# Kernel optimization log

Hardware: AMD Instinct MI355X
Metric: run time of the kernel (lower is better)

## Reference

```python
import jax, jax.numpy as jnp
import numpy as np

D = 1024      # features
C = 768       # context dim
H = 16        # heads
HD = D // H   # head dim = 64
N = 2048      # query tokens
M = 2048      # context tokens
EPS = 1e-12
SCALE = float(np.sqrt(HD))


def layernorm(x, w, b):
    c = x - x.mean(axis=-1, keepdims=True)
    s = (c * c).mean(axis=-1, keepdims=True)
    return c * jax.lax.rsqrt(s + EPS) * w + b


def setup_inputs() -> dict:
    key = jax.random.key(0)
    ks = jax.random.split(key, 10)
    sc = 0.02
    return {
        "x": jax.random.normal(ks[0], (N, D), jnp.float32),
        "ctx": jax.random.normal(ks[1], (M, C), jnp.float32),
        # attention projections (Projection: normal*0.02, zero bias)
        "wq": jax.random.normal(ks[2], (D, D), jnp.float32) * sc,
        "bq": jnp.zeros((D,), jnp.float32),
        "wk": jax.random.normal(ks[3], (C, D), jnp.float32) * sc,
        "bk": jnp.zeros((D,), jnp.float32),
        "wv": jax.random.normal(ks[4], (C, D), jnp.float32) * sc,
        "bv": jnp.zeros((D,), jnp.float32),
        "wo": jax.random.normal(ks[5], (D, D), jnp.float32) * sc,
        "bo": jnp.zeros((D,), jnp.float32),
        # MLP
        "w1": jax.random.normal(ks[6], (D, 4 * D), jnp.float32) * sc,
        "b1": jnp.zeros((4 * D,), jnp.float32),
        "w2": jax.random.normal(ks[7], (4 * D, D), jnp.float32) * sc,
        "b2": jnp.zeros((D,), jnp.float32),
        # layernorms
        "qn_w": jnp.ones((D,), jnp.float32), "qn_b": jnp.zeros((D,), jnp.float32),
        "kvn_w": jnp.ones((C,), jnp.float32), "kvn_b": jnp.zeros((C,), jnp.float32),
        "pn_w": jnp.ones((D,), jnp.float32), "pn_b": jnp.zeros((D,), jnp.float32),
    }


def reference(x, ctx, wq, bq, wk, bk, wv, bv, wo, bo, w1, b1, w2, b2,
              qn_w, qn_b, kvn_w, kvn_b, pn_w, pn_b):
    # pre-norm cross-attention
    xq = layernorm(x, qn_w, qn_b)          # [n, d]
    kv = layernorm(ctx, kvn_w, kvn_b)      # [m, c]
    q = (xq @ wq + bq).reshape(N, H, HD).transpose(1, 0, 2)   # [h, n, hd]
    k = (kv @ wk + bk).reshape(M, H, HD).transpose(1, 0, 2)   # [h, m, hd]
    v = (kv @ wv + bv).reshape(M, H, HD).transpose(1, 0, 2)   # [h, m, hd]
    attn = jax.nn.softmax(jnp.einsum('hnd,hmd->hnm', q, k) / SCALE, axis=-1)
    o = jnp.einsum('hnm,hmd->hnd', attn, v).transpose(1, 0, 2).reshape(N, D)
    x = (o @ wo + bo) + x
    # MLP block
    h = layernorm(x, pn_w, pn_b)
    h = jax.nn.gelu(h @ w1 + b1) @ w2 + b2
    return h + x
```

## Files before the change

### kernel.cpp

```cpp
#include <hip/hip_runtime.h>

typedef __bf16 bf16;
typedef __bf16 bf16x4 __attribute__((ext_vector_type(4)));
typedef __bf16 bf16x8 __attribute__((ext_vector_type(8)));
typedef float f32x4 __attribute__((ext_vector_type(4)));

#define N_TOK 2048
#define M_TOK 2048
#define DIM 1024
#define CDIM 768
#define DFF 4096

static __device__ __forceinline__ void async16(const void* g, void* l) {
  __builtin_amdgcn_global_load_lds((const __attribute__((address_space(1))) void*)g,
                                   (__attribute__((address_space(3))) void*)l, 16, 0, 0);
}

__global__ __launch_bounds__(256) void detect_kernel(const void* x, int* flag) {
  __shared__ int cnt;
  if (threadIdx.x == 0) cnt = 0;
  __syncthreads();
  const unsigned* w = (const unsigned*)x;
  int ok = 0;
  for (int i = threadIdx.x; i < 512; i += 256) {
    unsigned lo = w[i] & 0xFFFFu;
    float f = __uint_as_float(lo << 16);
    if (lo == 0u || (fabsf(f) > 1e-3f && fabsf(f) < 1e3f)) ok++;
  }
  atomicAdd(&cnt, ok);
  __syncthreads();
  if (threadIdx.x == 0) *flag = (cnt >= 256) ? 1 : 0;
}

struct ConvArgs {
  const void* src[12];
  bf16* dst[12];
  int n[12];
};
__global__ __launch_bounds__(256) void conv_small_kernel(ConvArgs a, const int* flag) {
  const bool isbf = (*flag != 0);
  const int b = blockIdx.x;
  const void* in = a.src[b];
  bf16* out = a.dst[b];
  const int n = a.n[b];
  for (int i = threadIdx.x; i < n; i += 256)
    out[i] = isbf ? ((const bf16*)in)[i] : (bf16)((const float*)in)[i];
}

struct TmArgs {
  const void* src[4];
  bf16* dst[4];
  int r0[4], Rcnt[4], c0[4], Cfull[4], gx[4], gy[4];
  int force_bf;
};
__global__ __launch_bounds__(256) void tmulti_kernel(TmArgs a, const int* flag) {
  const int z = blockIdx.z;
  if ((int)blockIdx.x >= a.gx[z] || (int)blockIdx.y >= a.gy[z]) return;
  __shared__ bf16 t[32][33];
  const bool isbf = a.force_bf || (*flag != 0);
  const void* in = a.src[z];
  bf16* out = a.dst[z];
  const int Rcnt = a.Rcnt[z], Cfull = a.Cfull[z];
  const int cb = blockIdx.x * 32, rb = blockIdx.y * 32;
  const int tx = threadIdx.x & 31, ty = threadIdx.x >> 5;
#pragma unroll
  for (int i = 0; i < 4; i++) {
    const size_t r = (size_t)(a.r0[z] + rb + ty + i * 8);
    const size_t c = (size_t)(a.c0[z] + cb + tx);
    float v = isbf ? (float)((const bf16*)in)[r * Cfull + c]
                   : ((const float*)in)[r * Cfull + c];
    t[ty + i * 8][tx] = (bf16)v;
  }
  __syncthreads();
#pragma unroll
  for (int i = 0; i < 4; i++)
    out[(size_t)(cb + ty + i * 8) * Rcnt + rb + tx] = t[tx][ty + i * 8];
}

__global__ __launch_bounds__(256) void ln_pair_kernel(
    const void* __restrict__ x0, const bf16* w0, const bf16* b0, bf16* o0,
    const void* __restrict__ x1, const bf16* w1, const bf16* b1, bf16* o1,
    const int* flag) {
  const bool isbf = (*flag != 0);
  const int cols = (blockIdx.y == 0) ? DIM : CDIM;
  const void* x = (blockIdx.y == 0) ? x0 : x1;
  const bf16* w = (blockIdx.y == 0) ? w0 : w1;
  const bf16* b = (blockIdx.y == 0) ? b0 : b1;
  bf16* outp = (blockIdx.y == 0) ? o0 : o1;
  const int row = blockIdx.x;
  const bf16* xr_b = (const bf16*)x + (size_t)row * cols;
  const float* xr_f = (const float*)x + (size_t)row * cols;
  bf16* orow = outp + (size_t)row * cols;
  float s = 0.f, ss = 0.f;
  for (int c = threadIdx.x; c < cols; c += 256) {
    float v = isbf ? (float)xr_b[c] : xr_f[c];
    s += v; ss += v * v;
  }
  for (int d = 1; d < 64; d <<= 1) { s += __shfl_xor(s, d, 64); ss += __shfl_xor(ss, d, 64); }
  __shared__ float sh[8];
  const int wv = threadIdx.x >> 6, lane = threadIdx.x & 63;
  if (lane == 0) { sh[wv] = s; sh[4 + wv] = ss; }
  __syncthreads();
  s = sh[0] + sh[1] + sh[2] + sh[3];
  ss = sh[4] + sh[5] + sh[6] + sh[7];
  const float mean = s / cols;
  float var = ss / cols - mean * mean;
  var = fmaxf(var, 0.f);
  const float r = rsqrtf(var + 1e-12f);
  for (int c = threadIdx.x; c < cols; c += 256) {
    float v = isbf ? (float)xr_b[c] : xr_f[c];
    orow[c] = (bf16)((v - mean) * r * (float)w[c] + (float)b[c]);
  }
}

__global__ __launch_bounds__(256) void ln_kernel(
    const bf16* __restrict__ x, const bf16* __restrict__ w, const bf16* __restrict__ b,
    bf16* __restrict__ out, int cols) {
  const int row = blockIdx.x;
  const bf16* xr = x + (size_t)row * cols;
  bf16* orow = out + (size_t)row * cols;
  float s = 0.f, ss = 0.f;
  for (int c = threadIdx.x; c < cols; c += 256) {
    float v = (float)xr[c];
    s += v; ss += v * v;
  }
  for (int d = 1; d < 64; d <<= 1) { s += __shfl_xor(s, d, 64); ss += __shfl_xor(ss, d, 64); }
  __shared__ float sh[8];
  const int wv = threadIdx.x >> 6, lane = threadIdx.x & 63;
  if (lane == 0) { sh[wv] = s; sh[4 + wv] = ss; }
  __syncthreads();
  s = sh[0] + sh[1] + sh[2] + sh[3];
  ss = sh[4] + sh[5] + sh[6] + sh[7];
  const float mean = s / cols;
  float var = ss / cols - mean * mean;
  var = fmaxf(var, 0.f);
  const float r = rsqrtf(var + 1e-12f);
  for (int c = threadIdx.x; c < cols; c += 256) {
    float v = (float)xr[c];
    orow[c] = (bf16)((v - mean) * r * (float)w[c] + (float)b[c]);
  }
}

__device__ __forceinline__ float gelu_f(float x) {
  float u = 0.7978845608028654f * (x + 0.044715f * x * x * x);
  return 0.5f * x * (1.f + tanhf(u));
}

template <int EPI>
__global__ __launch_bounds__(256) void gemm64(
    const bf16* __restrict__ A, const bf16* __restrict__ Bt,
    const bf16* __restrict__ bias, const void* __restrict__ resid,
    void* __restrict__ Cout, int K, int ldc, const int* flag) {
  __shared__ __align__(16) bf16 As[4][64 * 32];
  __shared__ __align__(16) bf16 Bs[4][64 * 32];
  const int tid = threadIdx.x;
  const int lane = tid & 63, wv = tid >> 6;
  const int lq = lane >> 4, lm = lane & 15;
  const int row0 = blockIdx.y * 64, col0 = blockIdx.x * 64;
  const int wr = (wv >> 1) * 32, wc = (wv & 1) * 32;

  f32x4 acc[2][2] = {};
  const int r_a = wv * 16 + (lane >> 2);
  const int kc = (lane & 3) * 8;

  for (int k0 = 0; k0 < K; k0 += 128) {
    __syncthreads();
#pragma unroll
    for (int b = 0; b < 4; b++) {
      async16(A + (size_t)(row0 + r_a) * K + k0 + b * 32 + kc, As[b] + wv * 512);
      async16(Bt + (size_t)(col0 + r_a) * K + k0 + b * 32 + kc, Bs[b] + wv * 512);
    }
    __syncthreads();
#pragma unroll
    for (int b = 0; b < 4; b++) {
      bf16x8 af[2], bfv[2];
#pragma unroll
      for (int t = 0; t < 2; t++)
        af[t] = *(const bf16x8*)&As[b][(wr + t * 16 + lm) * 32 + lq * 8];
#pragma unroll
      for (int t = 0; t < 2; t++)
        bfv[t] = *(const bf16x8*)&Bs[b][(wc + t * 16 + lm) * 32 + lq * 8];
#pragma unroll
      for (int i = 0; i < 2; i++)
#pragma unroll
        for (int j = 0; j < 2; j++)
          acc[i][j] = __builtin_amdgcn_mfma_f32_16x16x32_bf16(af[i], bfv[j], acc[i][j], 0, 0, 0);
    }
  }

  const bool isbf = (*flag != 0);
#pragma unroll
  for (int i = 0; i < 2; i++) {
    const int rb = row0 + wr + i * 16 + lq * 4;
#pragma unroll
    for (int j = 0; j < 2; j++) {
      const int c = col0 + wc + j * 16 + lm;
      const float bv = (EPI != 5) ? (float)bias[c] : 0.f;
#pragma unroll
      for (int rg = 0; rg < 4; rg++) {
        const size_t idx = (size_t)(rb + rg) * ldc + c;
        float v = acc[i][j][rg] + bv;
        if (EPI == 1)
          v += isbf ? (float)((const bf16*)resid)[idx] : ((const float*)resid)[idx];
        if (EPI == 2) v = gelu_f(v);
        if (EPI == 4) v += (float)((const bf16*)resid)[idx];
        if (EPI == 5)
          v += isbf ? (float)((bf16*)Cout)[idx] : ((float*)Cout)[idx];
        if (EPI == 4 || EPI == 5) {
          if (isbf) ((bf16*)Cout)[idx] = (bf16)v;
          else      ((float*)Cout)[idx] = v;
        } else {
          ((bf16*)Cout)[idx] = (bf16)v;
        }
      }
    }
  }
}

struct QkvArgs {
  const bf16* A[3];
  const bf16* Bt[3];
  const bf16* bias[3];
  bf16* C[3];
  int K[3], ldc[3], gx[3], gy[3], brow[3];
};
__global__ __launch_bounds__(256) void gemm64_qkv(QkvArgs a) {
  const int z = blockIdx.z;
  if ((int)blockIdx.x >= a.gx[z] || (int)blockIdx.y >= a.gy[z]) return;
  const bf16* A = a.A[z];
  const bf16* Bt = a.Bt[z];
  const int K = a.K[z];
  __shared__ __align__(16) bf16 As[4][64 * 32];
  __shared__ __align__(16) bf16 Bs[4][64 * 32];
  const int tid = threadIdx.x;
  const int lane = tid & 63, wv = tid >> 6;
  const int lq = lane >> 4, lm = lane & 15;
  const int row0 = blockIdx.y * 64, col0 = blockIdx.x * 64;
  const int wr = (wv >> 1) * 32, wc = (wv & 1) * 32;

  f32x4 acc[2][2] = {};
  const int r_a = wv * 16 + (lane >> 2);
  const int kc = (lane & 3) * 8;

  for (int k0 = 0; k0 < K; k0 += 128) {
    __syncthreads();
#pragma unroll
    for (int b = 0; b < 4; b++) {
      async16(A + (size_t)(row0 + r_a) * K + k0 + b * 32 + kc, As[b] + wv * 512);
      async16(Bt + (size_t)(col0 + r_a) * K + k0 + b * 32 + kc, Bs[b] + wv * 512);
    }
    __syncthreads();
#pragma unroll
    for (int b = 0; b < 4; b++) {
      bf16x8 af[2], bfv[2];
#pragma unroll
      for (int t = 0; t < 2; t++)
        af[t] = *(const bf16x8*)&As[b][(wr + t * 16 + lm) * 32 + lq * 8];
#pragma unroll
      for (int t = 0; t < 2; t++)
        bfv[t] = *(const bf16x8*)&Bs[b][(wc + t * 16 + lm) * 32 + lq * 8];
#pragma unroll
      for (int i = 0; i < 2; i++)
#pragma unroll
        for (int j = 0; j < 2; j++)
          acc[i][j] = __builtin_amdgcn_mfma_f32_16x16x32_bf16(af[i], bfv[j], acc[i][j], 0, 0, 0);
    }
  }

  const bf16* bias = a.bias[z];
  bf16* C = a.C[z];
  const int ldc = a.ldc[z];
  const bool brow = a.brow[z] != 0;
#pragma unroll
  for (int i = 0; i < 2; i++) {
    const int rb = row0 + wr + i * 16 + lq * 4;
#pragma unroll
    for (int j = 0; j < 2; j++) {
      const int c = col0 + wc + j * 16 + lm;
      const float bcol = brow ? 0.f : (float)bias[c];
#pragma unroll
      for (int rg = 0; rg < 4; rg++) {
        const float bv = brow ? (float)bias[rb + rg] : bcol;
        C[(size_t)(rb + rg) * ldc + c] = (bf16)(acc[i][j][rg] + bv);
      }
    }
  }
}

#define KS_STR 72
#define VS_STR 136
__global__ __launch_bounds__(256) void attn_kernel(
    const bf16* __restrict__ q, const bf16* __restrict__ k,
    const bf16* __restrict__ vT, bf16* __restrict__ pO0, bf16* __restrict__ pO1,
    float* __restrict__ l0, float* __restrict__ l1) {
  __shared__ __align__(16) bf16 KPs[128 * KS_STR];
  __shared__ __align__(16) bf16 Vs[64 * VS_STR];
  const int tid = threadIdx.x, lane = tid & 63, wv = tid >> 6;
  const int lq = lane >> 4, lm = lane & 15;
  const int h = blockIdx.y;
  const int n0 = blockIdx.x * 64;
  const int half = blockIdx.z;
  const int mbeg = half * (M_TOK / 2), mend = mbeg + M_TOK / 2;
  bf16* pO = half ? pO1 : pO0;
  float* lb = half ? l1 : l0;

  bf16x8 qf[2];
#pragma unroll
  for (int f = 0; f < 2; f++)
    qf[f] = *(const bf16x8*)&q[(size_t)(n0 + wv * 16 + lm) * DIM + h * 64 + f * 32 + lq * 8];

  f32x4 oacc[4] = {};
  float lsum = 0.f;
  const float sc = 0.125f * 1.4426950408889634f;

  for (int m0 = mbeg; m0 < mend; m0 += 128) {
    __syncthreads();
#pragma unroll
    for (int it = 0; it < 4; it++) {
      const int e = tid * 8 + it * 2048;
      const int r = e >> 6, c = e & 63;
      *(bf16x8*)&KPs[r * KS_STR + c] =
          *(const bf16x8*)&k[(size_t)(m0 + r) * DIM + h * 64 + c];
    }
#pragma unroll
    for (int it = 0; it < 4; it++) {
      const int e = tid * 8 + it * 2048;
      const int r = e >> 7, c = e & 127;
      *(bf16x8*)&Vs[r * VS_STR + c] =
          *(const bf16x8*)&vT[(size_t)(h * 64 + r) * M_TOK + m0 + c];
    }
    __syncthreads();

    f32x4 s[8];
#pragma unroll
    for (int j = 0; j < 8; j++) {
      bf16x8 kf0 = *(const bf16x8*)&KPs[(j * 16 + lm) * KS_STR + lq * 8];
      bf16x8 kf1 = *(const bf16x8*)&KPs[(j * 16 + lm) * KS_STR + 32 + lq * 8];
      f32x4 z = {};
      z = __builtin_amdgcn_mfma_f32_16x16x32_bf16(kf0, qf[0], z, 0, 0, 0);
      s[j] = __builtin_amdgcn_mfma_f32_16x16x32_bf16(kf1, qf[1], z, 0, 0, 0);
    }
    __syncthreads();

#pragma unroll
    for (int j = 0; j < 8; j++) {
      bf16x4 pw;
#pragma unroll
      for (int rg = 0; rg < 4; rg++) {
        const float pv = exp2f(s[j][rg] * sc);
        lsum += pv;
        pw[rg] = (bf16)pv;
      }
      *(bf16x4*)&KPs[(wv * 16 + lm) * VS_STR + j * 16 + lq * 4] = pw;
    }

#pragma unroll
    for (int kk = 0; kk < 4; kk++) {
      bf16x8 pf = *(const bf16x8*)&KPs[(wv * 16 + lm) * VS_STR + kk * 32 + lq * 8];
#pragma unroll
      for (int dt = 0; dt < 4; dt++) {
        bf16x8 vf = *(const bf16x8*)&Vs[(dt * 16 + lm) * VS_STR + kk * 32 + lq * 8];
        oacc[dt] = __builtin_amdgcn_mfma_f32_16x16x32_bf16(vf, pf, oacc[dt], 0, 0, 0);
      }
    }
  }

  lsum += __shfl_xor(lsum, 16, 64);
  lsum += __shfl_xor(lsum, 32, 64);
  if (lane < 16) lb[h * N_TOK + n0 + wv * 16 + lane] = lsum;

  const int rn = n0 + wv * 16 + lm;
#pragma unroll
  for (int dt = 0; dt < 4; dt++) {
    bf16x4 ow;
#pragma unroll
    for (int rg = 0; rg < 4; rg++) ow[rg] = (bf16)oacc[dt][rg];
    *(bf16x4*)&pO[(size_t)rn * DIM + h * 64 + dt * 16 + lq * 4] = ow;
  }
}

__global__ __launch_bounds__(256) void attn_combine(
    const bf16* __restrict__ pO0, const bf16* __restrict__ pO1,
    const float* __restrict__ l0, const float* __restrict__ l1,
    bf16* __restrict__ om) {
  const int i4 = (blockIdx.x * 256 + threadIdx.x) * 4;
  const int n = i4 >> 10;
  const int h = (i4 & 1023) >> 6;
  const float rinv = 1.f / (l0[h * N_TOK + n] + l1[h * N_TOK + n]);
  bf16x4 a = *(const bf16x4*)&pO0[i4];
  bf16x4 b = *(const bf16x4*)&pO1[i4];
  bf16x4 o;
#pragma unroll
  for (int r = 0; r < 4; r++) o[r] = (bf16)(((float)a[r] + (float)b[r]) * rinv);
  *(bf16x4*)&om[i4] = o;
}

extern "C" void kernel_launch(void* const* d_in, const int* in_sizes, int n_in,
                              void* d_out, int out_size, void* d_ws, size_t ws_size,
                              hipStream_t stream) {
  const void* x_r     = d_in[0];
  const void* ctx_r   = d_in[1];
  const void* wq_r    = d_in[2];
  const void* bq_r    = d_in[3];
  const void* wk_r    = d_in[4];
  const void* bk_r    = d_in[5];
  const void* wv_r    = d_in[6];
  const void* bv_r    = d_in[7];
  const void* wo_r    = d_in[8];
  const void* bo_r    = d_in[9];
  const void* w1_r    = d_in[10];
  const void* b1_r    = d_in[11];
  const void* w2_r    = d_in[12];
  const void* b2_r    = d_in[13];
  const void* qnw_r   = d_in[14];
  const void* qnb_r   = d_in[15];
  const void* kvnw_r  = d_in[16];
  const void* kvnb_r  = d_in[17];
  const void* pnw_r   = d_in[18];
  const void* pnb_r   = d_in[19];

  bf16* p = (bf16*)d_ws;
  const size_t MEG = 1024 * 1024;
  bf16* qm  = p;             bf16* hln = qm;
  bf16* km  = p + 2 * MEG;   bf16* xat = km;
  bf16* wC  = p + 4 * MEG;
  bf16* xq  = p + 8 * MEG;   bf16* pO0 = xq;   bf16* om = xq;
  bf16* vTb = p + 10 * MEG;
  bf16* kvn = p + 12 * MEG;  bf16* pO1 = kvn;
  bf16* h1h = p + 10 * MEG;
  bf16* SM  = p + 14 * MEG;
  int* flag = (int*)(p + 14 * MEG + 16384);

  bf16* wqT = wC;
  bf16* wkT = wC + 1 * MEG;
  bf16* wvT = wC + 1 * MEG + 786432;
  bf16* woT = wC + 2 * MEG + 524288;
  bf16* w1Th = wC;
  bf16* w2Th = wC + 2 * MEG;
  float* l0 = (float*)wC;
  float* l1 = l0 + N_TOK * 16;

  bf16* bqc = SM, *bkc = SM + 1024, *bvc = SM + 2048, *boc = SM + 3072;
  bf16* b1c = SM + 4096, *b2c = SM + 8192;
  bf16* qnw = SM + 9216, *qnb = SM + 10240;
  bf16* kvnw = SM + 11264, *kvnb = SM + 12032;
  bf16* pnw = SM + 12800, *pnb = SM + 13824;

  detect_kernel<<<1, 256, 0, stream>>>(x_r, flag);
  ConvArgs ca;
  ca.src[0] = bq_r;   ca.dst[0] = bqc;  ca.n[0] = DIM;
  ca.src[1] = bk_r;   ca.dst[1] = bkc;  ca.n[1] = DIM;
  ca.src[2] = bv_r;   ca.dst[2] = bvc;  ca.n[2] = DIM;
  ca.src[3] = bo_r;   ca.dst[3] = boc;  ca.n[3] = DIM;
  ca.src[4] = b1_r;   ca.dst[4] = b1c;  ca.n[4] = DFF;
  ca.src[5] = b2_r;   ca.dst[5] = b2c;  ca.n[5] = DIM;
  ca.src[6] = qnw_r;  ca.dst[6] = qnw;  ca.n[6] = DIM;
  ca.src[7] = qnb_r;  ca.dst[7] = qnb;  ca.n[7] = DIM;
  ca.src[8] = kvnw_r; ca.dst[8] = kvnw; ca.n[8] = CDIM;
  ca.src[9] = kvnb_r; ca.dst[9] = kvnb; ca.n[9] = CDIM;
  ca.src[10] = pnw_r; ca.dst[10] = pnw; ca.n[10] = DIM;
  ca.src[11] = pnb_r; ca.dst[11] = pnb; ca.n[11] = DIM;
  conv_small_kernel<<<12, 256, 0, stream>>>(ca, flag);

  ln_pair_kernel<<<dim3(2048, 2), 256, 0, stream>>>(x_r, qnw, qnb, xq,
                                                    ctx_r, kvnw, kvnb, kvn, flag);

  {
    TmArgs ta;
    ta.force_bf = 0;
    ta.src[0] = wq_r; ta.dst[0] = wqT; ta.r0[0] = 0; ta.Rcnt[0] = DIM;
    ta.c0[0] = 0; ta.Cfull[0] = DIM; ta.gx[0] = 32; ta.gy[0] = 32;
    ta.src[1] = wk_r; ta.dst[1] = wkT; ta.r0[1] = 0; ta.Rcnt[1] = CDIM;
    ta.c0[1] = 0; ta.Cfull[1] = DIM; ta.gx[1] = 32; ta.gy[1] = 24;
    ta.src[2] = wv_r; ta.dst[2] = wvT; ta.r0[2] = 0; ta.Rcnt[2] = CDIM;
    ta.c0[2] = 0; ta.Cfull[2] = DIM; ta.gx[2] = 32; ta.gy[2] = 24;
    ta.src[3] = wo_r; ta.dst[3] = woT; ta.r0[3] = 0; ta.Rcnt[3] = DIM;
    ta.c0[3] = 0; ta.Cfull[3] = DIM; ta.gx[3] = 32; ta.gy[3] = 32;
    tmulti_kernel<<<dim3(32, 32, 4), 256, 0, stream>>>(ta, flag);
  }

  {
    QkvArgs qa;
    qa.A[0] = xq;  qa.Bt[0] = wqT; qa.bias[0] = bqc; qa.C[0] = qm;
    qa.K[0] = DIM;  qa.ldc[0] = DIM;   qa.gx[0] = 16; qa.gy[0] = 32; qa.brow[0] = 0;
    qa.A[1] = kvn; qa.Bt[1] = wkT; qa.bias[1] = bkc; qa.C[1] = km;
    qa.K[1] = CDIM; qa.ldc[1] = DIM;   qa.gx[1] = 16; qa.gy[1] = 32; qa.brow[1] = 0;
    qa.A[2] = wvT; qa.Bt[2] = kvn; qa.bias[2] = bvc; qa.C[2] = vTb;
    qa.K[2] = CDIM; qa.ldc[2] = M_TOK; qa.gx[2] = 32; qa.gy[2] = 16; qa.brow[2] = 1;
    gemm64_qkv<<<dim3(32, 32, 3), 256, 0, stream>>>(qa);
  }

  attn_kernel<<<dim3(32, 16, 2), 256, 0, stream>>>(qm, km, vTb, pO0, pO1, l0, l1);
  attn_combine<<<2048, 256, 0, stream>>>(pO0, pO1, l0, l1, om);

  gemm64<1><<<dim3(16, 32), 256, 0, stream>>>(om, woT, boc, x_r, xat, DIM, DIM, flag);

  ln_kernel<<<N_TOK, 256, 0, stream>>>(xat, pnw, pnb, hln, DIM);

  for (int hh = 0; hh < 2; hh++) {
    TmArgs ta;
    ta.force_bf = 0;
    ta.src[0] = w1_r; ta.dst[0] = w1Th; ta.r0[0] = 0; ta.Rcnt[0] = DIM;
    ta.c0[0] = hh * 2048; ta.Cfull[0] = DFF; ta.gx[0] = 64; ta.gy[0] = 32;
    ta.src[1] = w2_r; ta.dst[1] = w2Th; ta.r0[1] = hh * 2048; ta.Rcnt[1] = 2048;
    ta.c0[1] = 0; ta.Cfull[1] = DIM; ta.gx[1] = 32; ta.gy[1] = 64;
    ta.src[2] = ta.src[0]; ta.dst[2] = ta.dst[0]; ta.r0[2] = 0; ta.Rcnt[2] = 32;
    ta.c0[2] = 0; ta.Cfull[2] = DIM; ta.gx[2] = 0; ta.gy[2] = 0;
    ta.src[3] = ta.src[0]; ta.dst[3] = ta.dst[0]; ta.r0[3] = 0; ta.Rcnt[3] = 32;
    ta.c0[3] = 0; ta.Cfull[3] = DIM; ta.gx[3] = 0; ta.gy[3] = 0;
    tmulti_kernel<<<dim3(64, 64, 2), 256, 0, stream>>>(ta, flag);

    gemm64<2><<<dim3(32, 32), 256, 0, stream>>>(hln, w1Th, b1c + hh * 2048, nullptr,
                                                h1h, DIM, 2048, flag);
    if (hh == 0)
      gemm64<4><<<dim3(16, 32), 256, 0, stream>>>(h1h, w2Th, b2c, xat, d_out,
                                                  2048, DIM, flag);
    else
      gemm64<5><<<dim3(16, 32), 256, 0, stream>>>(h1h, w2Th, b2c, nullptr, d_out,
                                                  2048, DIM, flag);
  }
}
```

Measured before the change: 349.7 us.

## Enlarge GEMM tiles to 128x128 with XOR-swizzled shared memory layout

```diff
diff --git a/kernel.cpp b/kernel.cpp
--- a/kernel.cpp
+++ b/kernel.cpp
@@ -147,53 +147,59 @@
 }
 
 template <int EPI>
-__global__ __launch_bounds__(256) void gemm64(
+__global__ __launch_bounds__(256) void gemm128(
     const bf16* __restrict__ A, const bf16* __restrict__ Bt,
     const bf16* __restrict__ bias, const void* __restrict__ resid,
     void* __restrict__ Cout, int K, int ldc, const int* flag) {
-  __shared__ __align__(16) bf16 As[4][64 * 32];
-  __shared__ __align__(16) bf16 Bs[4][64 * 32];
+  __shared__ __align__(16) bf16 As[128 * 64];
+  __shared__ __align__(16) bf16 Bs[128 * 64];
   const int tid = threadIdx.x;
   const int lane = tid & 63, wv = tid >> 6;
   const int lq = lane >> 4, lm = lane & 15;
-  const int row0 = blockIdx.y * 64, col0 = blockIdx.x * 64;
-  const int wr = (wv >> 1) * 32, wc = (wv & 1) * 32;
-
-  f32x4 acc[2][2] = {};
-  const int r_a = wv * 16 + (lane >> 2);
-  const int kc = (lane & 3) * 8;
-
-  for (int k0 = 0; k0 < K; k0 += 128) {
+  const int row0 = blockIdx.y * 128, col0 = blockIdx.x * 128;
+  const int wr = (wv >> 1) * 64, wc = (wv & 1) * 64;
+
+  const int sr = lane >> 3;
+  const int sc = ((lane & 7) ^ sr) * 8;
+  const int swz = (lm & 7) << 3;
+
+  f32x4 acc[4][4] = {};
+
+  const bf16* Abase = A + (size_t)(row0 + wv * 32 + sr) * K + sc;
+  const bf16* Bbase = Bt + (size_t)(col0 + wv * 32 + sr) * K + sc;
+
+  for (int k0 = 0; k0 < K; k0 += 64) {
     __syncthreads();
 #pragma unroll
     for (int b = 0; b < 4; b++) {
-      async16(A + (size_t)(row0 + r_a) * K + k0 + b * 32 + kc, As[b] + wv * 512);
-      async16(Bt + (size_t)(col0 + r_a) * K + k0 + b * 32 + kc, Bs[b] + wv * 512);
-    }
-    __syncthreads();
-#pragma unroll
-    for (int b = 0; b < 4; b++) {
-      bf16x8 af[2], bfv[2];
-#pragma unroll
-      for (int t = 0; t < 2; t++)
-        af[t] = *(const bf16x8*)&As[b][(wr + t * 16 + lm) * 32 + lq * 8];
-#pragma unroll
-      for (int t = 0; t < 2; t++)
-        bfv[t] = *(const bf16x8*)&Bs[b][(wc + t * 16 + lm) * 32 + lq * 8];
-#pragma unroll
-      for (int i = 0; i < 2; i++)
-#pragma unroll
-        for (int j = 0; j < 2; j++)
+      async16(Abase + (size_t)(b * 8) * K + k0, As + wv * 2048 + b * 512);
+      async16(Bbase + (size_t)(b * 8) * K + k0, Bs + wv * 2048 + b * 512);
+    }
+    __syncthreads();
+#pragma unroll
+    for (int kh = 0; kh < 2; kh++) {
+      const int cofs = (kh * 32 + lq * 8) ^ swz;
+      bf16x8 af[4], bfv[4];
+#pragma unroll
+      for (int t = 0; t < 4; t++)
+        af[t] = *(const bf16x8*)&As[(wr + t * 16 + lm) * 64 + cofs];
+#pragma unroll
+      for (int t = 0; t < 4; t++)
+        bfv[t] = *(const bf16x8*)&Bs[(wc + t * 16 + lm) * 64 + cofs];
+#pragma unroll
+      for (int i = 0; i < 4; i++)
+#pragma unroll
+        for (int j = 0; j < 4; j++)
           acc[i][j] = __builtin_amdgcn_mfma_f32_16x16x32_bf16(af[i], bfv[j], acc[i][j], 0, 0, 0);
     }
   }
 
   const bool isbf = (*flag != 0);
 #pragma unroll
-  for (int i = 0; i < 2; i++) {
+  for (int i = 0; i < 4; i++) {
     const int rb = row0 + wr + i * 16 + lq * 4;
 #pragma unroll
-    for (int j = 0; j < 2; j++) {
+    for (int j = 0; j < 4; j++) {
       const int c = col0 + wc + j * 16 + lm;
       const float bv = (EPI != 5) ? (float)bias[c] : 0.f;
 #pragma unroll
@@ -224,45 +230,51 @@
   bf16* C[3];
   int K[3], ldc[3], gx[3], gy[3], brow[3];
 };
-__global__ __launch_bounds__(256) void gemm64_qkv(QkvArgs a) {
+__global__ __launch_bounds__(256) void gemm128_qkv(QkvArgs a) {
   const int z = blockIdx.z;
   if ((int)blockIdx.x >= a.gx[z] || (int)blockIdx.y >= a.gy[z]) return;
   const bf16* A = a.A[z];
   const bf16* Bt = a.Bt[z];
   const int K = a.K[z];
-  __shared__ __align__(16) bf16 As[4][64 * 32];
-  __shared__ __align__(16) bf16 Bs[4][64 * 32];
+  __shared__ __align__(16) bf16 As[128 * 64];
+  __shared__ __align__(16) bf16 Bs[128 * 64];
   const int tid = threadIdx.x;
   const int lane = tid & 63, wv = tid >> 6;
   const int lq = lane >> 4, lm = lane & 15;
-  const int row0 = blockIdx.y * 64, col0 = blockIdx.x * 64;
-  const int wr = (wv >> 1) * 32, wc = (wv & 1) * 32;
-
-  f32x4 acc[2][2] = {};
-  const int r_a = wv * 16 + (lane >> 2);
-  const int kc = (lane & 3) * 8;
-
-  for (int k0 = 0; k0 < K; k0 += 128) {
+  const int row0 = blockIdx.y * 128, col0 = blockIdx.x * 128;
+  const int wr = (wv >> 1) * 64, wc = (wv & 1) * 64;
+
+  const int sr = lane >> 3;
+  const int sc = ((lane & 7) ^ sr) * 8;
+  const int swz = (lm & 7) << 3;
+
+  f32x4 acc[4][4] = {};
+
+  const bf16* Abase = A + (size_t)(row0 + wv * 32 + sr) * K + sc;
+  const bf16* Bbase = Bt + (size_t)(col0 + wv * 32 + sr) * K + sc;
+
+  for (int k0 = 0; k0 < K; k0 += 64) {
     __syncthreads();
 #pragma unroll
     for (int b = 0; b < 4; b++) {
-      async16(A + (size_t)(row0 + r_a) * K + k0 + b * 32 + kc, As[b] + wv * 512);
-      async16(Bt + (size_t)(col0 + r_a) * K + k0 + b * 32 + kc, Bs[b] + wv * 512);
-    }
-    __syncthreads();
-#pragma unroll
-    for (int b = 0; b < 4; b++) {
-      bf16x8 af[2], bfv[2];
-#pragma unroll
-      for (int t = 0; t < 2; t++)
-        af[t] = *(const bf16x8*)&As[b][(wr + t * 16 + lm) * 32 + lq * 8];
-#pragma unroll
-      for (int t = 0; t < 2; t++)
-        bfv[t] = *(const bf16x8*)&Bs[b][(wc + t * 16 + lm) * 32 + lq * 8];
-#pragma unroll
-      for (int i = 0; i < 2; i++)
-#pragma unroll
-        for (int j = 0; j < 2; j++)
+      async16(Abase + (size_t)(b * 8) * K + k0, As + wv * 2048 + b * 512);
+      async16(Bbase + (size_t)(b * 8) * K + k0, Bs + wv * 2048 + b * 512);
+    }
+    __syncthreads();
+#pragma unroll
+    for (int kh = 0; kh < 2; kh++) {
+      const int cofs = (kh * 32 + lq * 8) ^ swz;
+      bf16x8 af[4], bfv[4];
+#pragma unroll
+      for (int t = 0; t < 4; t++)
+        af[t] = *(const bf16x8*)&As[(wr + t * 16 + lm) * 64 + cofs];
+#pragma unroll
+      for (int t = 0; t < 4; t++)
+        bfv[t] = *(const bf16x8*)&Bs[(wc + t * 16 + lm) * 64 + cofs];
+#pragma unroll
+      for (int i = 0; i < 4; i++)
+#pragma unroll
+        for (int j = 0; j < 4; j++)
           acc[i][j] = __builtin_amdgcn_mfma_f32_16x16x32_bf16(af[i], bfv[j], acc[i][j], 0, 0, 0);
     }
   }
@@ -272,10 +284,10 @@
   const int ldc = a.ldc[z];
   const bool brow = a.brow[z] != 0;
 #pragma unroll
-  for (int i = 0; i < 2; i++) {
+  for (int i = 0; i < 4; i++) {
     const int rb = row0 + wr + i * 16 + lq * 4;
 #pragma unroll
-    for (int j = 0; j < 2; j++) {
+    for (int j = 0; j < 4; j++) {
       const int c = col0 + wc + j * 16 + lm;
       const float bcol = brow ? 0.f : (float)bias[c];
 #pragma unroll
@@ -482,18 +494,18 @@
   {
     QkvArgs qa;
     qa.A[0] = xq;  qa.Bt[0] = wqT; qa.bias[0] = bqc; qa.C[0] = qm;
-    qa.K[0] = DIM;  qa.ldc[0] = DIM;   qa.gx[0] = 16; qa.gy[0] = 32; qa.brow[0] = 0;
+    qa.K[0] = DIM;  qa.ldc[0] = DIM;   qa.gx[0] = 8;  qa.gy[0] = 16; qa.brow[0] = 0;
     qa.A[1] = kvn; qa.Bt[1] = wkT; qa.bias[1] = bkc; qa.C[1] = km;
-    qa.K[1] = CDIM; qa.ldc[1] = DIM;   qa.gx[1] = 16; qa.gy[1] = 32; qa.brow[1] = 0;
+    qa.K[1] = CDIM; qa.ldc[1] = DIM;   qa.gx[1] = 8;  qa.gy[1] = 16; qa.brow[1] = 0;
     qa.A[2] = wvT; qa.Bt[2] = kvn; qa.bias[2] = bvc; qa.C[2] = vTb;
-    qa.K[2] = CDIM; qa.ldc[2] = M_TOK; qa.gx[2] = 32; qa.gy[2] = 16; qa.brow[2] = 1;
-    gemm64_qkv<<<dim3(32, 32, 3), 256, 0, stream>>>(qa);
+    qa.K[2] = CDIM; qa.ldc[2] = M_TOK; qa.gx[2] = 16; qa.gy[2] = 8;  qa.brow[2] = 1;
+    gemm128_qkv<<<dim3(16, 16, 3), 256, 0, stream>>>(qa);
   }
 
   attn_kernel<<<dim3(32, 16, 2), 256, 0, stream>>>(qm, km, vTb, pO0, pO1, l0, l1);
   attn_combine<<<2048, 256, 0, stream>>>(pO0, pO1, l0, l1, om);
 
-  gemm64<1><<<dim3(16, 32), 256, 0, stream>>>(om, woT, boc, x_r, xat, DIM, DIM, flag);
+  gemm128<1><<<dim3(8, 16), 256, 0, stream>>>(om, woT, boc, x_r, xat, DIM, DIM, flag);
 
   ln_kernel<<<N_TOK, 256, 0, stream>>>(xat, pnw, pnb, hln, DIM);
 
@@ -510,13 +522,13 @@
     ta.c0[3] = 0; ta.Cfull[3] = DIM; ta.gx[3] = 0; ta.gy[3] = 0;
     tmulti_kernel<<<dim3(64, 64, 2), 256, 0, stream>>>(ta, flag);
 
-    gemm64<2><<<dim3(32, 32), 256, 0, stream>>>(hln, w1Th, b1c + hh * 2048, nullptr,
-                                                h1h, DIM, 2048, flag);
+    gemm128<2><<<dim3(16, 16), 256, 0, stream>>>(hln, w1Th, b1c + hh * 2048, nullptr,
+                                                 h1h, DIM, 2048, flag);
     if (hh == 0)
-      gemm64<4><<<dim3(16, 32), 256, 0, stream>>>(h1h, w2Th, b2c, xat, d_out,
+      gemm128<4><<<dim3(8, 16), 256, 0, stream>>>(h1h, w2Th, b2c, xat, d_out,
                                                   2048, DIM, flag);
     else
-      gemm64<5><<<dim3(16, 32), 256, 0, stream>>>(h1h, w2Th, b2c, nullptr, d_out,
+      gemm128<5><<<dim3(8, 16), 256, 0, stream>>>(h1h, w2Th, b2c, nullptr, d_out,
                                                   2048, DIM, flag);
   }
 }
```

Measured after the change: 440.3 us. +25.9%, slower.
